# Kernel optimization log

Measured on AMD Instinct MI355X. Metric: run time of the kernel, lower is better.

The kernel has to match this reference:

```python
import math
import jax, jax.numpy as jnp
from jax import lax
import numpy as np

N_IMG = 2
C = 128
IMG_H, IMG_W = 512, 1024
STRIDES = (4, 8, 16, 32, 64)
SIZES = (32.0, 64.0, 128.0, 256.0, 512.0)
RATIOS = (0.5, 1.0, 2.0)
A = len(RATIOS)
PRE_NMS_TOPK = 2000    # pre_nms_topk[self.training] with training=True
POST_NMS_TOPK = 1000   # post_nms_topk[self.training]
NMS_THRESH = 0.7
BATCH_PER_IMG = 256
POS_FRAC = 0.5
MIN_BOX_SIZE = 0.0
SCALE_CLAMP = math.log(1000.0 / 16.0)
MATCH_LOW, MATCH_HIGH = 0.3, 0.7


def cell_anchors(size):
    rs = jnp.asarray(RATIOS, jnp.float32)
    area = size * size
    w = jnp.sqrt(area / rs)
    h = w * rs
    return jnp.stack([-w / 2, -h / 2, w / 2, h / 2], axis=1)  # [A,4]


def level_anchors(H, W, stride, size):
    ca = cell_anchors(size)
    sx = jnp.arange(W, dtype=jnp.float32) * stride
    sy = jnp.arange(H, dtype=jnp.float32) * stride
    yy, xx = jnp.meshgrid(sy, sx, indexing="ij")
    shifts = jnp.stack([xx, yy, xx, yy], axis=-1).reshape(-1, 4)  # [H*W,4]
    return (shifts[:, None, :] + ca[None, :, :]).reshape(-1, 4)  # [H*W*A,4]


def pairwise_iou(a, b):
    lt = jnp.maximum(a[:, None, :2], b[None, :, :2])
    rb = jnp.minimum(a[:, None, 2:], b[None, :, 2:])
    wh = jnp.clip(rb - lt, 0.0)
    inter = wh[..., 0] * wh[..., 1]
    area_a = (a[:, 2] - a[:, 0]) * (a[:, 3] - a[:, 1])
    area_b = (b[:, 2] - b[:, 0]) * (b[:, 3] - b[:, 1])
    union = area_a[:, None] + area_b[None, :] - inter
    return jnp.where(inter > 0, inter / union, 0.0)


def get_deltas(src, tgt):
    sw = src[..., 2] - src[..., 0]; sh = src[..., 3] - src[..., 1]
    scx = src[..., 0] + 0.5 * sw;   scy = src[..., 1] + 0.5 * sh
    tw = tgt[..., 2] - tgt[..., 0]; th = tgt[..., 3] - tgt[..., 1]
    tcx = tgt[..., 0] + 0.5 * tw;   tcy = tgt[..., 1] + 0.5 * th
    return jnp.stack([(tcx - scx) / sw, (tcy - scy) / sh,
                      jnp.log(tw / sw), jnp.log(th / sh)], axis=-1)


def apply_deltas(deltas, boxes):
    w = boxes[..., 2] - boxes[..., 0]; h = boxes[..., 3] - boxes[..., 1]
    cx = boxes[..., 0] + 0.5 * w;      cy = boxes[..., 1] + 0.5 * h
    dx, dy = deltas[..., 0], deltas[..., 1]
    dw = jnp.minimum(deltas[..., 2], SCALE_CLAMP)
    dh = jnp.minimum(deltas[..., 3], SCALE_CLAMP)
    pcx = dx * w + cx; pcy = dy * h + cy
    pw = jnp.exp(dw) * w; ph = jnp.exp(dh) * h
    return jnp.stack([pcx - 0.5 * pw, pcy - 0.5 * ph,
                      pcx + 0.5 * pw, pcy + 0.5 * ph], axis=-1)


def conv(x, w, b):
    y = lax.conv_general_dilated(x, w, (1, 1), "SAME",
                                 dimension_numbers=("NCHW", "OIHW", "NCHW"))
    return y + b[None, :, None, None]


def rpn_forward_flat(feats, conv_w, conv_b, obj_w, obj_b, delta_w, delta_b):
    anchors, logits, deltas = [], [], []
    for (stride, size), f in zip(zip(STRIDES, SIZES), feats):
        N, _, H, W = f.shape
        h = jax.nn.relu(conv(f, conv_w, conv_b))
        lg = conv(h, obj_w, obj_b)       # [N,A,H,W]
        dl = conv(h, delta_w, delta_b)   # [N,4A,H,W]
        logits.append(lg.transpose(0, 2, 3, 1).reshape(N, -1))                     # [N,HWA]
        deltas.append(dl.reshape(N, A, 4, H, W).transpose(0, 3, 4, 1, 2).reshape(N, -1, 4))
        anchors.append(level_anchors(H, W, stride, size))
    return anchors, logits, deltas


def label_and_sample(gt_b, key, anchors_all):
    iou = pairwise_iou(gt_b, anchors_all)                 # [G,R]
    matched_idxs = jnp.argmax(iou, axis=0)
    matched_vals = jnp.max(iou, axis=0)
    labels = jnp.where(matched_vals >= MATCH_HIGH, 1,
             jnp.where(matched_vals >= MATCH_LOW, -1, 0))
    highest = jnp.max(iou, axis=1)                        # per-gt best IoU
    lq = jnp.any((iou == highest[:, None]) & (highest[:, None] > 0), axis=0)
    labels = jnp.where(lq, 1, labels)                     # allow_low_quality_matches
    R = labels.shape[0]
    kf, kb = jax.random.split(key)
    fg = labels == 1; bg = labels == 0
    num_fg = jnp.minimum(fg.sum(), int(POS_FRAC * BATCH_PER_IMG))
    num_bg = jnp.minimum(bg.sum(), BATCH_PER_IMG - num_fg)
    def pick(mask, k, num):
        pri = jnp.where(mask, jax.random.uniform(k, (R,)), jnp.inf)
        rank = jnp.argsort(jnp.argsort(pri))
        return rank < num
    sel_fg = pick(fg, kf, num_fg)
    sel_bg = pick(bg, kb, num_bg)
    labels = jnp.where(sel_fg, 1, jnp.where(sel_bg, 0, -1))
    return labels, gt_b[matched_idxs]


def losses_fn(anchors_all, logits_cat, deltas_cat, gt_labels, matched_gt):
    fg = (gt_labels == 1).astype(logits_cat.dtype)          # [N,R]
    gt_deltas = get_deltas(anchors_all[None], matched_gt)   # [N,R,4]
    loc = jnp.sum(jnp.abs(deltas_cat - gt_deltas) * fg[..., None])  # smooth_l1, beta=0
    valid = (gt_labels >= 0).astype(logits_cat.dtype)
    x = logits_cat
    bce = jnp.maximum(x, 0.0) - x * fg + jnp.log1p(jnp.exp(-jnp.abs(x)))
    cls = jnp.sum(bce * valid)
    norm = float(BATCH_PER_IMG) * logits_cat.shape[0]
    return jnp.stack([cls / norm, loc / norm])


def nms_keep(boxes, valid):
    # boxes are sorted by descending score; greedy suppression.
    K = boxes.shape[0]
    iou = pairwise_iou(boxes, boxes)
    idx = jnp.arange(K)
    def body(i, keep):
        sup = (iou[i] > NMS_THRESH) & (idx > i) & keep[i]
        return keep & ~sup
    return lax.fori_loop(0, K, body, valid)


def predict_proposals(anchors, logits, deltas):
    lvl_boxes, lvl_scores = [], []
    for anc, lg, dl in zip(anchors, logits, deltas):
        boxes = apply_deltas(dl, anc[None])             # [N,R_l,4]
        k = min(PRE_NMS_TOPK, lg.shape[1])
        ts, ti = lax.top_k(lg, k)                       # [N,k]
        tb = jnp.take_along_axis(boxes, ti[..., None], axis=1)
        tb = jnp.stack([jnp.clip(tb[..., 0], 0.0, IMG_W), jnp.clip(tb[..., 1], 0.0, IMG_H),
                        jnp.clip(tb[..., 2], 0.0, IMG_W), jnp.clip(tb[..., 3], 0.0, IMG_H)], -1)
        valid = ((tb[..., 2] - tb[..., 0]) > MIN_BOX_SIZE) & ((tb[..., 3] - tb[..., 1]) > MIN_BOX_SIZE)
        keep = jax.vmap(nms_keep)(tb, valid)
        lvl_boxes.append(tb)
        lvl_scores.append(jnp.where(keep, ts, -jnp.inf))
    all_b = jnp.concatenate(lvl_boxes, axis=1)
    all_s = jnp.concatenate(lvl_scores, axis=1)
    fs, fi = lax.top_k(all_s, POST_NMS_TOPK)
    fb = jnp.take_along_axis(all_b, fi[..., None], axis=1)
    return fb, fs


def setup_inputs() -> dict:
    key = jax.random.key(0)
    ks = jax.random.split(key, 12)
    out = {}
    for i, s in enumerate(STRIDES):
        out[f"feat_p{i+2}"] = jax.random.normal(ks[i], (N_IMG, C, IMG_H // s, IMG_W // s), jnp.float32)
    G = 32
    wh_scale = jnp.asarray([IMG_W, IMG_H], jnp.float32)
    cxy = jax.random.uniform(ks[5], (N_IMG, G, 2)) * wh_scale
    wh = 32.0 + jax.random.uniform(ks[6], (N_IMG, G, 2)) * 224.0
    x1y1 = jnp.clip(cxy - wh / 2, 0.0)
    x2y2 = jnp.maximum(jnp.minimum(cxy + wh / 2, wh_scale), x1y1 + 1.0)
    out["gt_boxes"] = jnp.concatenate([x1y1, x2y2], axis=-1)
    out["conv_w"] = 0.01 * jax.random.normal(ks[7], (C, C, 3, 3), jnp.float32)
    out["conv_b"] = jnp.zeros((C,), jnp.float32)
    out["obj_w"] = 0.01 * jax.random.normal(ks[8], (A, C, 1, 1), jnp.float32)
    out["obj_b"] = jnp.zeros((A,), jnp.float32)
    out["delta_w"] = 0.01 * jax.random.normal(ks[9], (4 * A, C, 1, 1), jnp.float32)
    out["delta_b"] = jnp.zeros((4 * A,), jnp.float32)
    return out


def reference(feat_p2, feat_p3, feat_p4, feat_p5, feat_p6, gt_boxes,
              conv_w, conv_b, obj_w, obj_b, delta_w, delta_b):
    feats = [feat_p2, feat_p3, feat_p4, feat_p5, feat_p6]
    anchors, logits, deltas = rpn_forward_flat(feats, conv_w, conv_b, obj_w, obj_b, delta_w, delta_b)
    anchors_all = jnp.concatenate(anchors, axis=0)      # [R,4]
    logits_cat = jnp.concatenate(logits, axis=1)        # [N,R]
    deltas_cat = jnp.concatenate(deltas, axis=1)        # [N,R,4]
    keys = jax.random.split(jax.random.key(42), gt_boxes.shape[0])
    gt_labels, matched_gt = jax.vmap(label_and_sample, in_axes=(0, 0, None))(gt_boxes, keys, anchors_all)
    losses = losses_fn(anchors_all, logits_cat, deltas_cat, gt_labels, matched_gt)
    prop_boxes, prop_scores = predict_proposals(
        anchors,
        [lax.stop_gradient(l) for l in logits],
        [lax.stop_gradient(d) for d in deltas])
    return prop_boxes, prop_scores, losses
```

## Files before the change

kernel.cpp:

```cpp
#include <hip/hip_runtime.h>
#include <stdint.h>
#include <math.h>


#define R_TOT   130944
#define HALF_R  65472
#define TOTK    7920
#define SCALE_CLAMP 4.135166556742356

__host__ __device__ inline void threefry(uint32_t k0, uint32_t k1,
                                         uint32_t x0, uint32_t x1,
                                         uint32_t* o0, uint32_t* o1)
{
  uint32_t ks[3]; ks[0]=k0; ks[1]=k1; ks[2]=k0^k1^0x1BD11BDAu;
  x0 += ks[0]; x1 += ks[1];
  const uint32_t rot0[4] = {13u,15u,26u,6u};
  const uint32_t rot1[4] = {17u,29u,16u,24u};
  for (int i = 0; i < 5; i++){
    const uint32_t* rot = (i & 1) ? rot1 : rot0;
    for (int q = 0; q < 4; q++){
      x0 += x1;
      x1 = (x1 << rot[q]) | (x1 >> (32u - rot[q]));
      x1 ^= x0;
    }
    x0 += ks[(i+1)%3];
    x1 += ks[(i+2)%3] + (uint32_t)(i+1);
  }
  *o0 = x0; *o1 = x1;
}

__device__ inline unsigned long long mono64(double v){
  unsigned long long b = (unsigned long long)__double_as_longlong(v);
  return (b & 0x8000000000000000ull) ? ~b : (b | 0x8000000000000000ull);
}

__device__ __forceinline__ double iou_cf(double g0,double g1,double g2,double g3,
                                         double a0,double a1,double a2,double a3){
  #pragma clang fp contract(off)
  double lt0 = fmax(g0,a0), lt1 = fmax(g1,a1);
  double rb0 = fmin(g2,a2), rb1 = fmin(g3,a3);
  double w = rb0-lt0; if (w<0.0) w=0.0;
  double h = rb1-lt1; if (h<0.0) h=0.0;
  double inter = w*h;
  double aa = (g2-g0)*(g3-g1);
  double ab = (a2-a0)*(a3-a1);
  double uni = aa+ab-inter;
  return inter>0.0 ? inter/uni : 0.0;
}

__device__ __forceinline__ void anchor_of(int r, double* o){
  #pragma clang fp contract(off)
  const int    base[5]={0,98304,122880,129024,130560};
  const int    Wl[5]  ={256,128,64,32,16};
  const double strd[5]={4.0,8.0,16.0,32.0,64.0};
  const double size[5]={32.0,64.0,128.0,256.0,512.0};
  const double ratio[3]={0.5,1.0,2.0};
  int l=0; while (l<4 && r>=base[l+1]) l++;
  int rr=r-base[l]; int pix=rr/3; int a=rr-pix*3;
  int x=pix%Wl[l], y=pix/Wl[l];
  double w=sqrt(size[l]*size[l]/ratio[a]);
  double h=w*ratio[a];
  double sx=(double)x*strd[l], sy=(double)y*strd[l];
  o[0]=sx-0.5*w; o[1]=sy-0.5*h; o[2]=sx+0.5*w; o[3]=sy+0.5*h;
}

__device__ __forceinline__ void decode_box(int ridx, const double* __restrict__ d,
                                           double* __restrict__ o){
  double a[4]; anchor_of(ridx,a);
  double w=a[2]-a[0], h=a[3]-a[1];
  double cx=a[0]+0.5*w, cy=a[1]+0.5*h;
  double dw=fmin(d[2],SCALE_CLAMP), dh=fmin(d[3],SCALE_CLAMP);
  double pcx=d[0]*w+cx, pcy=d[1]*h+cy;
  double pw=exp(dw)*w, ph=exp(dh)*h;
  double x1=pcx-0.5*pw, y1=pcy-0.5*ph;
  double x2=pcx+0.5*pw, y2=pcy+0.5*ph;
  o[0]=fmin(fmax(x1,0.0),1024.0); o[1]=fmin(fmax(y1,0.0),512.0);
  o[2]=fmin(fmax(x2,0.0),1024.0); o[3]=fmin(fmax(y2,0.0),512.0);
}

__device__ inline void bitonic_desc(double* sv, int* si, int M, int tid, int nthr){
  for (int k=2;k<=M;k<<=1)
    for (int j=k>>1;j>0;j>>=1){
      __syncthreads();
      for (int i=tid;i<M;i+=nthr){
        int ixj=i^j;
        if (ixj>i){
          double va=sv[i], vb=sv[ixj]; int ia=si[i], ib=si[ixj];
          bool before = (va>vb) || (va==vb && ia<ib);
          bool up = ((i&k)==0);
          if (up ? !before : before){ sv[i]=vb; sv[ixj]=va; si[i]=ib; si[ixj]=ia; }
        }
      }
    }
  __syncthreads();
}

__device__ inline void bitonic_asc_u(uint32_t* sk, int* si, int M, int tid, int nthr){
  for (int k=2;k<=M;k<<=1)
    for (int j=k>>1;j>0;j>>=1){
      __syncthreads();
      for (int i=tid;i<M;i+=nthr){
        int ixj=i^j;
        if (ixj>i){
          uint32_t ka=sk[i], kb=sk[ixj]; int ia=si[i], ib=si[ixj];
          bool before = (ka<kb) || (ka==kb && ia<ib);
          bool up = ((i&k)==0);
          if (up ? !before : before){ sk[i]=kb; sk[ixj]=ka; si[i]=ib; si[ixj]=ia; }
        }
      }
    }
  __syncthreads();
}

__global__ __launch_bounds__(256) void k_pre(const float* __restrict__ cw,
    float* __restrict__ cwTf, uint32_t* __restrict__ ub,
    const float* __restrict__ gt, unsigned long long* __restrict__ highest,
    uint32_t kf00,uint32_t kf01,uint32_t kb00,uint32_t kb01,
    uint32_t kf10,uint32_t kf11,uint32_t kb10,uint32_t kb11)
{
  const int bx=blockIdx.x, tid=threadIdx.x;
  if (bx < 576){
    int o = bx*256 + tid;
    if (o >= 147456) return;
    int cc = o & 127; int t = o >> 7;
    int k9 = t % 9;  int ci = t / 9;
    cwTf[(size_t)(ci*9+k9)*128 + cc] = cw[(size_t)cc*1152 + ci*9 + k9];
  } else if (bx < 1599){
    int j = (bx-576)*256 + tid;
    if (j >= 2*R_TOT) return;
    int slot = j / HALF_R; int t = j - slot*HALF_R;
    uint32_t k0,k1;
    if      (slot==0){k0=kf00;k1=kf01;}
    else if (slot==1){k0=kb00;k1=kb01;}
    else if (slot==2){k0=kf10;k1=kf11;}
    else             {k0=kb10;k1=kb11;}
    uint32_t o0,o1;
    threefry(k0,k1,(uint32_t)t,(uint32_t)(t+HALF_R),&o0,&o1);
    ub[(size_t)slot*R_TOT+t]=o0;
    ub[(size_t)slot*R_TOT+t+HALF_R]=o1;
  } else {
    __shared__ double gts[128];
    __shared__ unsigned long long lmax[32];
    const int gb=bx-1599;
    const int img=gb>>6, b=gb&63;
    if (tid<128) gts[tid]=(double)gt[img*128+tid];
    if (tid<32) lmax[tid]=0ull;
    __syncthreads();
    double gm[32];
    #pragma unroll
    for (int g=0;g<32;g++) gm[g]=0.0;
    for (int r=b*256+tid; r<R_TOT; r+=64*256){
      double a[4]; anchor_of(r,a);
      #pragma unroll
      for (int g=0;g<32;g++){
        double v=iou_cf(gts[g*4],gts[g*4+1],gts[g*4+2],gts[g*4+3],a[0],a[1],a[2],a[3]);
        gm[g]=fmax(gm[g],v);
      }
    }
    #pragma unroll
    for (int g=0;g<32;g++){
      double v=gm[g];
      #pragma unroll
      for (int off=1; off<64; off<<=1) v=fmax(v,__shfl_xor(v,off));
      if ((tid&63)==0) atomicMax(&lmax[g],(unsigned long long)__double_as_longlong(v));
    }
    __syncthreads();
    if (tid<32) atomicMax(&highest[img*32+tid], lmax[tid]);
  }
}

#define CTH 4
#define CTW 8

__global__ __launch_bounds__(256,3) void k_conv_label(
    const float* __restrict__ f2, const float* __restrict__ f3,
    const float* __restrict__ f4, const float* __restrict__ f5,
    const float* __restrict__ f6,
    const float* __restrict__ cwTf, const float* __restrict__ cb,
    const float* __restrict__ ow, const float* __restrict__ ob,
    const float* __restrict__ dwt, const float* __restrict__ dbt,
    double* __restrict__ logits, double* __restrict__ dpred,
    const float* __restrict__ gt, const unsigned long long* __restrict__ highest,
    int* __restrict__ prelab, int* __restrict__ matched,
    int* __restrict__ labels, int* __restrict__ counts)
{
  __shared__ double fshd[4][6][12];
  __shared__ __align__(16) char ush[33792];
  float*  wshF = (float*)ush;
  double* hshp = (double*)ush;
  __shared__ float hw[15*128];
  __shared__ float hb[15];

  const int tid=threadIdx.x;

  if (blockIdx.x >= 2728){
    double* gts=(double*)ush;
    double* hg =(double*)(ush+1024);
    int* wfg=(int*)(ush+1280); int* wbg=(int*)(ush+1296);
    const int lb=blockIdx.x-2728;
    const int img=lb>>9, blk=lb&511;
    if (tid<128) gts[tid]=(double)gt[img*128+tid];
    if (tid<32)  hg[tid]=__longlong_as_double((long long)highest[img*32+tid]);
    __syncthreads();
    int r=blk*256+tid;
    const bool ok=(r<R_TOT);
    int lab=-1, bi=0;
    if (ok){
      double a[4]; anchor_of(r,a);
      double best=-1.0; bool lq=false;
      #pragma unroll
      for (int g=0;g<32;g++){
        double v=iou_cf(gts[g*4],gts[g*4+1],gts[g*4+2],gts[g*4+3],a[0],a[1],a[2],a[3]);
        if (v>best){ best=v; bi=g; }
        if (hg[g]>0.0 && v==hg[g]) lq=true;
      }
      lab = lq ? 1 : (best>=0.7 ? 1 : (best>=0.3 ? -1 : 0));
      prelab [(size_t)img*R_TOT+r]=lab;
      matched[(size_t)img*R_TOT+r]=bi;
      labels [(size_t)img*R_TOT+r]=-1;
    }
    unsigned long long bf=__ballot(ok && lab==1);
    unsigned long long bb=__ballot(ok && lab==0);
    const int wid=tid>>6, lane=tid&63;
    if (lane==0){ wfg[wid]=__popcll(bf); wbg[wid]=__popcll(bb); }
    __syncthreads();
    if (tid==0){
      int fcnt=wfg[0]+wfg[1]+wfg[2]+wfg[3];
      int bcnt=wbg[0]+wbg[1]+wbg[2]+wbg[3];
      if (fcnt) atomicAdd(&counts[img*2+0],fcnt);
      if (bcnt) atomicAdd(&counts[img*2+1],bcnt);
    }
    return;
  }

  const int cumt[6]={0,2048,2560,2688,2720,2728};
  const int Hs[5]={128,64,32,16,8}, Wl[5]={256,128,64,32,16};
  const int rbs[5]={0,98304,122880,129024,130560};
  const int lgx[5]={5,4,3,2,1};

  int bid=blockIdx.x;
  int lvl=0;
  while (lvl<4 && bid>=cumt[lvl+1]) lvl++;
  int t=bid-cumt[lvl];
  const int img=t&1; const int tt=t>>1;
  const int H=Hs[lvl], W=Wl[lvl], rbase=rbs[lvl];
  const int tx=tt&((1<<lgx[lvl])-1), ty=tt>>lgx[lvl];
  const int x0=tx*CTW, y0=ty*CTH;
  const float* f = lvl==0?f2: lvl==1?f3: lvl==2?f4: lvl==3?f5: f6;

  for (int i=tid;i<15*128;i+=256){
    int o=i>>7, c=i&127;
    hw[i]=(o<3)?ow[o*128+c]:dwt[(o-3)*128+c];
  }
  if (tid<15) hb[tid]=(tid<3)?ob[tid]:dbt[tid-3];

  const int c=tid&127, half=tid>>7;
  double acc[16];
  #pragma unroll
  for (int i=0;i<16;i++) acc[i]=0.0;

  const float* fimg = f + (size_t)img*128*H*W;

  const bool fin_act = (tid < 240);
  int ci_f=0,dy_f=0,dx_f=0; bool fin_valid=false;
  const float* fptr=fimg;
  if (fin_act){
    ci_f=tid/60; int rem=tid-ci_f*60; dy_f=rem/10; dx_f=rem-dy_f*10;
    int y=y0-1+dy_f, x=x0-1+dx_f;
    fin_valid = (y>=0&&y<H&&x>=0&&x<W);
    fptr = fimg + (size_t)ci_f*H*W + (fin_valid ? ((size_t)y*W+x) : 0);
  }
  const size_t fstep=(size_t)4*H*W;
  const float2* wsrc=(const float2*)cwTf;

  float fin_pf=0.f; float2 wpf[9];
  if (fin_act){ fin_pf = fin_valid ? *fptr : 0.f; fptr += fstep; }
  #pragma unroll
  for (int j2=0;j2<9;j2++) wpf[j2]=wsrc[tid+j2*256];

  for (int ci0=0; ci0<128; ci0+=4){
    __syncthreads();
    if (fin_act) fshd[ci_f][dy_f][dx_f]=(double)fin_pf;
    { float2* wdst=(float2*)wshF;
      #pragma unroll
      for (int j2=0;j2<9;j2++) wdst[tid+j2*256]=wpf[j2]; }
    if (ci0+4<128){
      if (fin_act){ fin_pf = fin_valid ? *fptr : 0.f; fptr += fstep; }
      const float2* wn = wsrc + (size_t)(ci0+4)*576;
      #pragma unroll
      for (int j2=0;j2<9;j2++) wpf[j2]=wn[tid+j2*256];
    }
    __syncthreads();
    #pragma unroll
    for (int ci=0;ci<4;ci++){
      double w9d[9];
      #pragma unroll
      for (int k=0;k<9;k++) w9d[k]=(double)wshF[(ci*9+k)*128 + c];
      #pragma unroll
      for (int irl=0;irl<4;irl++){
        int ir=half*2+irl;
        double rowb[10];
        #pragma unroll
        for (int q=0;q<10;q++) rowb[q]=fshd[ci][ir][q];
        #pragma unroll
        for (int orl=0;orl<2;orl++){
          int ky=irl-orl;
          if (ky<0||ky>2) continue;
          #pragma unroll
          for (int px=0;px<8;px++){
            double s=acc[orl*8+px];
            #pragma unroll
            for (int kx=0;kx<3;kx++) s += w9d[ky*3+kx]*rowb[px+kx];
            acc[orl*8+px]=s;
          }
        }
      }
    }
  }
  __syncthreads();
  double bc=(double)cb[c];
  #pragma unroll
  for (int pp=0;pp<16;pp++){
    double hv=acc[pp]+bc; if (hv<0.0) hv=0.0;
    hshp[c*33+(half*16+pp)]=hv;
  }
  __syncthreads();
  for (int j=tid;j<480;j+=256){
    int o=j>>5, p=j&31;
    int py=p>>3, px=p&7;
    double s=(double)hb[o];
    for (int c2=0;c2<128;c2++) s += (double)hw[o*128+c2]*hshp[c2*33+p];
    int gy=y0+py, gx=x0+px;
    long long pix=(long long)gy*W+gx;
    size_t rb=(size_t)rbase+(size_t)pix*3;
    if (o<3) logits[(size_t)img*R_TOT+rb+o]=s;
    else { int a=(o-3)>>2, jj=(o-3)&3; dpred[((size_t)img*R_TOT+rb+a)*4+jj]=s; }
  }
}

__global__ __launch_bounds__(1024) void k_mid2(const uint32_t* __restrict__ ub,
    const int* __restrict__ prelab, const int* __restrict__ counts,
    int* __restrict__ labels,
    const double* __restrict__ logits, const double* __restrict__ dpred,
    double* __restrict__ allS, double* __restrict__ allB)
{
  __shared__ __align__(16) char buf[49152];
  __shared__ int hist[256];
  __shared__ int sI0, sI1; __shared__ unsigned long long sT;
  __shared__ int cnt;
  const int tid=threadIdx.x;

  if (blockIdx.x < 4){
    uint32_t* skey=(uint32_t*)buf; int* sidx=(int*)(buf+16384);
    const int img=blockIdx.x>>1, cls=blockIdx.x&1;
    const int cfg=counts[img*2+0], cbg=counts[img*2+1];
    const int num_fg=cfg<128?cfg:128;
    const int cap_bg=256-num_fg;
    const int num=cls?(cbg<cap_bg?cbg:cap_bg):num_fg;
    if (num<=0) return;
    const int want=cls?0:1;
    const int sel=want;
    const uint32_t* u=ub+(size_t)(img*2+cls)*R_TOT;
    const int* pl=prelab+(size_t)img*R_TOT;
    int* lab=labels+(size_t)img*R_TOT;

    for (int b=tid;b<256;b+=1024) hist[b]=0;
    if (tid==0) cnt=0;
    __syncthreads();
    for (int r=tid;r<R_TOT;r+=1024){
      int plr = pl[r];
      uint32_t key = u[r]>>9;
      if (plr==want) atomicAdd(&hist[key>>15],1);
    }
    __syncthreads();
    if (tid==0){
      int cum=0,b=0;
      for (;b<255;b++){ int hh=hist[b]; if (cum+hh>=num) break; cum+=hh; }
      sI0=b; sI1=num-cum;
    }
    __syncthreads();
    const uint32_t bsel=(uint32_t)sI0; const int kneed=sI1;
    for (int r=tid;r<R_TOT;r+=1024){
      int plr = pl[r];
      uint32_t key = u[r]>>9;
      if (plr==want){
        uint32_t t8=key>>15;
        if (t8<bsel) lab[r]=sel;
        else if (t8==bsel){ int p=atomicAdd(&cnt,1); if (p<4096){ skey[p]=key; sidx[p]=r; } }
      }
    }
    __syncthreads();
    int n=cnt<4096?cnt:4096;
    for (int i=tid;i<4096;i+=1024) if (i>=n){ skey[i]=0xFFFFFFFFu; sidx[i]=0x7FFFFFFF; }
    bitonic_asc_u(skey,sidx,4096,tid,1024);
    int take = kneed<n?kneed:n;
    for (int i=tid;i<take;i+=1024) lab[sidx[i]]=sel;
  } else {
    double* sv=(double*)buf; int* si=(int*)(buf+32768);
    const int Rl[5]   ={98304,24576,6144,1536,384};
    const int kl[5]   ={2000,2000,2000,1536,384};
    const int lbase[5]={0,98304,122880,129024,130560};
    const int loff[5] ={0,2000,4000,6000,7536};
    const int bb=blockIdx.x-4;
    const int lvl=bb%5, img=bb/5;
    const int Rn=Rl[lvl], K=kl[lvl];
    const double* lg=logits+(size_t)img*R_TOT+lbase[lvl];

    unsigned long long chosen=0; int kneed=K;
    for (int ps=7; ps>=6; --ps){
      int shift=ps*8;
      for (int b=tid;b<256;b+=1024) hist[b]=0;
      __syncthreads();
      for (int r=tid;r<Rn;r+=1024){
        unsigned long long ik=~mono64(lg[r]);
        bool okp=(ps==7)||((ik>>(shift+8))==(chosen>>(shift+8)));
        if (okp) atomicAdd(&hist[(int)((ik>>shift)&255)],1);
      }
      __syncthreads();
      if (tid==0){
        int cum=0,b=0;
        for (;b<255;b++){ int hh=hist[b]; if (cum+hh>=kneed) break; cum+=hh; }
        sT=chosen|((unsigned long long)b<<shift); sI1=kneed-cum;
      }
      __syncthreads();
      chosen=sT; kneed=sI1;
      __syncthreads();
    }
    const unsigned long long lim = chosen | 0xFFFFFFFFFFFFull;
    if (tid==0) cnt=0;
    __syncthreads();
    for (int r=tid;r<Rn;r+=1024){
      unsigned long long ik=~mono64(lg[r]);
      if (ik<=lim){ int p=atomicAdd(&cnt,1); if (p<4096){ sv[p]=lg[r]; si[p]=r; } }
    }
    __syncthreads();
    int n=cnt<4096?cnt:4096;
    for (int i=tid;i<4096;i+=1024) if (i>=n){ sv[i]=-HUGE_VAL; si[i]=0x7FFFFFFF; }
    bitonic_desc(sv,si,4096,tid,1024);
    for (int j=tid;j<K;j+=1024){
      double v=sv[j]; int r=si[j];
      size_t slot=(size_t)img*TOTK+loff[lvl]+j;
      allS[slot]=v;
      int ridx=lbase[lvl]+r;
      double bx[4];
      decode_box(ridx, dpred+((size_t)img*R_TOT+ridx)*4, bx);
      allB[slot*4+0]=bx[0]; allB[slot*4+1]=bx[1]; allB[slot*4+2]=bx[2]; allB[slot*4+3]=bx[3];
    }
  }
}

__global__ __launch_bounds__(256) void k_mid3(const double* __restrict__ allB,
    unsigned long long* __restrict__ msk,
    const double* __restrict__ logits, const double* __restrict__ dpred,
    const float* __restrict__ gt, const int* __restrict__ labels,
    const int* __restrict__ matched, double* __restrict__ part)
{
  const int bx=blockIdx.x, tid=threadIdx.x;
  if (bx < 1980){
    __shared__ double Bsh[8000];
    const int kl[5]  ={2000,2000,2000,1536,384};
    const int loff[5]={0,2000,4000,6000,7536};
    const int rbc[6] ={0,250,500,750,942,990};
    const int img = bx/990; int t = bx - img*990;
    int lvl=0; while (lvl<4 && t>=rbc[lvl+1]) lvl++;
    const int i0=(t-rbc[lvl])*8;
    const int K=kl[lvl]; const int nw=(K+63)>>6;
    const double* B=allB+(size_t)(img*TOTK+loff[lvl])*4;
    for (int q=tid;q<K*4;q+=256) Bsh[q]=B[q];
    __syncthreads();
    const int wv=tid>>6, lane=tid&63;
    for (int rr=0;rr<8;rr++){
      int i=i0+rr;
      if (i>=K) break;
      const double bi0=Bsh[i*4],bi1=Bsh[i*4+1],bi2=Bsh[i*4+2],bi3=Bsh[i*4+3];
      const double areai=(bi2-bi0)*(bi3-bi1);
      for (int w=wv;w<nw;w+=4){
        int j=w*64+lane;
        bool pred=false;
        if (j<K && j>i){
          double a0=Bsh[j*4],a1=Bsh[j*4+1],a2=Bsh[j*4+2],a3=Bsh[j*4+3];
          double lt0=fmax(bi0,a0), lt1=fmax(bi1,a1);
          double rb0=fmin(bi2,a2), rb1=fmin(bi3,a3);
          double ww=rb0-lt0; if (ww<0.0) ww=0.0;
          double hh=rb1-lt1; if (hh<0.0) hh=0.0;
          double inter=ww*hh;
          double uni=areai+(a2-a0)*(a3-a1)-inter;
          double iou=inter>0.0?inter/uni:0.0;
          pred = iou>0.7;
        }
        unsigned long long m=__ballot(pred);
        if (lane==0) msk[((size_t)img*TOTK+loff[lvl]+i)*32+w]=m;
      }
    }
  } else {
    const int bid2=bx-1980;
    double cls=0.0, loc=0.0;
    for (int idx=bid2*256+tid; idx<2*R_TOT; idx+=256*256){
      int l=labels[idx];
      if (l<0) continue;
      double x=logits[idx];
      double fgv=(l==1)?1.0:0.0;
      cls += fmax(x,0.0)-x*fgv+log1p(exp(-fabs(x)));
      if (l==1){
        int img=idx/R_TOT, r=idx-img*R_TOT;
        double a[4]; anchor_of(r,a);
        int m=matched[idx];
        const float* g=gt+img*128+m*4;
        double sw=a[2]-a[0], sh=a[3]-a[1];
        double scx=a[0]+0.5*sw, scy=a[1]+0.5*sh;
        double tw=(double)g[2]-(double)g[0], th=(double)g[3]-(double)g[1];
        double tcx=(double)g[0]+0.5*tw, tcy=(double)g[1]+0.5*th;
        double d0=(tcx-scx)/sw, d1=(tcy-scy)/sh;
        double d2=log(tw/sw), d3=log(th/sh);
        const double* dp=dpred+(size_t)idx*4;
        loc += fabs(dp[0]-d0)+fabs(dp[1]-d1)+fabs(dp[2]-d2)+fabs(dp[3]-d3);
      }
    }
    __shared__ double sc[256], sl[256];
    sc[tid]=cls; sl[tid]=loc; __syncthreads();
    for (int s=128;s>0;s>>=1){
      if (tid<s){ sc[tid]+=sc[tid+s]; sl[tid]+=sl[tid+s]; }
      __syncthreads();
    }
    if (tid==0){ part[bid2*2]=sc[0]; part[bid2*2+1]=sl[0]; }
  }
}

#define NMS_LD(BUF, BASE) do{ \
  _Pragma("unroll") \
  for (int j_=0;j_<16;j_++){ int i_=(BASE)+j_; \
    BUF[j_] = (lane<nw && i_<K) ? M[(size_t)i_*32+lane] : 0ull; } \
}while(0)
#define NMS_PR(BUF, BASE) do{ \
  _Pragma("unroll") \
  for (int j_=0;j_<16;j_++){ int i_=(BASE)+j_; \
    if (i_<K){ unsigned long long kw_=__shfl(keep,(i_>>6)); \
      if ((kw_>>(i_&63))&1ull) keep &= ~BUF[j_]; } } \
}while(0)

__global__ void k_nmsscan(const double* __restrict__ allB, double* __restrict__ allS,
    const unsigned long long* __restrict__ msk){
  const int kl[5]  ={2000,2000,2000,1536,384};
  const int loff[5]={0,2000,4000,6000,7536};
  const int lvl=blockIdx.x, img=blockIdx.y;
  const int K=kl[lvl], off=loff[lvl], nw=(K+63)>>6;
  const int lane=threadIdx.x;
  const double* B=allB+(size_t)(img*TOTK+off)*4;
  const unsigned long long* M=msk+((size_t)img*TOTK+off)*32;
  unsigned long long keep=0ull;
  if (lane<nw){
    for (int b=0;b<64;b++){
      int j=lane*64+b;
      if (j<K){
        double x1=B[(size_t)j*4],y1=B[(size_t)j*4+1],x2=B[(size_t)j*4+2],y2=B[(size_t)j*4+3];
        if ((x2-x1)>0.0 && (y2-y1)>0.0) keep|=(1ull<<b);
      }
    }
  }
  unsigned long long Abuf[16], Bbuf[16];
  NMS_LD(Abuf, 0);
  for (int base=0; base<K; base+=32){
    NMS_LD(Bbuf, base+16);
    NMS_PR(Abuf, base);
    NMS_LD(Abuf, base+32);
    NMS_PR(Bbuf, base+16);
  }
  if (lane<nw){
    for (int b=0;b<64;b++){
      int j=lane*64+b;
      if (j<K && !((keep>>b)&1ull))
        allS[(size_t)img*TOTK+off+j]=-HUGE_VAL;
    }
  }
}

__global__ __launch_bounds__(1024) void k_final(const double* __restrict__ allS,
    const double* __restrict__ allB, const double* __restrict__ part,
    float* __restrict__ out){
  const int tid=threadIdx.x;
  if (blockIdx.x==2){
    __shared__ double sc[256], sl[256];
    if (tid<256){ sc[tid]=part[tid*2]; sl[tid]=part[tid*2+1]; }
    __syncthreads();
    for (int s=128;s>0;s>>=1){
      if (tid<s){ sc[tid]+=sc[tid+s]; sl[tid]+=sl[tid+s]; }
      __syncthreads();
    }
    if (tid==0){ out[10000]=(float)(sc[0]/512.0); out[10001]=(float)(sl[0]/512.0); }
    return;
  }
  const int img=blockIdx.x;
  const double* sarr=allS+(size_t)img*TOTK;
  __shared__ int hist[256];
  __shared__ unsigned long long sT; __shared__ int sK;
  __shared__ double sv[4096]; __shared__ int si[4096]; __shared__ int cnt;

  unsigned long long chosen=0; int kneed=1000;
  for (int ps=7; ps>=0; --ps){
    int shift=ps*8;
    for (int b=tid;b<256;b+=1024) hist[b]=0;
    __syncthreads();
    for (int r=tid;r<TOTK;r+=1024){
      unsigned long long ik=~mono64(sarr[r]);
      bool okp=(ps==7)||((ik>>(shift+8))==(chosen>>(shift+8)));
      if (okp) atomicAdd(&hist[(int)((ik>>shift)&255)],1);
    }
    __syncthreads();
    if (tid==0){
      int cum=0,b=0;
      for (;b<255;b++){ int hh=hist[b]; if (cum+hh>=kneed) break; cum+=hh; }
      sT=chosen|((unsigned long long)b<<shift); sK=kneed-cum;
    }
    __syncthreads();
    chosen=sT; kneed=sK;
    __syncthreads();
  }
  if (tid==0) cnt=0;
  __syncthreads();
  for (int r=tid;r<TOTK;r+=1024){
    unsigned long long ik=~mono64(sarr[r]);
    if (ik<=chosen){ int p=atomicAdd(&cnt,1); if (p<4096){ sv[p]=sarr[r]; si[p]=r; } }
  }
  __syncthreads();
  int n=cnt<4096?cnt:4096;
  for (int i=tid;i<4096;i+=1024) if (i>=n){ sv[i]=-HUGE_VAL; si[i]=0x7FFFFFFF; }
  bitonic_desc(sv,si,4096,tid,1024);
  for (int j=tid;j<1000;j+=1024){
    out[8000+img*1000+j]=(float)sv[j];
    int idx=si[j];
    const double* b=allB+((size_t)img*TOTK+idx)*4;
    float* ob=out+((size_t)img*1000+j)*4;
    ob[0]=(float)b[0]; ob[1]=(float)b[1]; ob[2]=(float)b[2]; ob[3]=(float)b[3];
  }
}

extern "C" void kernel_launch(void* const* d_in, const int* in_sizes, int n_in,
                              void* d_out, int out_size, void* d_ws, size_t ws_size,
                              hipStream_t stream)
{
  (void)in_sizes; (void)n_in; (void)out_size;
  const float* feats[5];
  for (int i=0;i<5;i++) feats[i]=(const float*)d_in[i];
  const float* gt =(const float*)d_in[5];
  const float* cw =(const float*)d_in[6];
  const float* cb =(const float*)d_in[7];
  const float* ow =(const float*)d_in[8];
  const float* ob =(const float*)d_in[9];
  const float* dwt=(const float*)d_in[10];
  const float* dbt=(const float*)d_in[11];
  float* out=(float*)d_out;

  char* p=(char*)d_ws;
  auto carve=[&](size_t nbytes)->char*{ char* q=p; p += (nbytes+255)&~(size_t)255; return q; };
  double* logits =(double*)carve(2ull*R_TOT*8);
  double* dpred  =(double*)carve(2ull*R_TOT*4*8);
  float* cwTf    =(float*)carve(147456ull*4);
  uint32_t* ub   =(uint32_t*)carve(4ull*R_TOT*4);
  int* prelab    =(int*)carve(2ull*R_TOT*4);
  int* matched   =(int*)carve(2ull*R_TOT*4);
  int* labels    =(int*)carve(2ull*R_TOT*4);
  unsigned long long* highest=(unsigned long long*)carve(2*32*8);
  int* counts    =(int*)carve(256);
  double* allS   =(double*)carve(2ull*TOTK*8);
  double* allB   =(double*)carve(2ull*TOTK*4*8);
  unsigned long long* msk=(unsigned long long*)carve(2ull*TOTK*32*8);
  double* part   =(double*)carve(256*2*8);
  if ((size_t)(p-(char*)d_ws) > ws_size) return;

  hipMemsetAsync(highest, 0, 768, stream);

  uint32_t a0,b0,a1,b1;
  threefry(0u,42u,0u,2u,&a0,&b0);
  threefry(0u,42u,1u,3u,&a1,&b1);
  uint32_t kf00,kf01,kb00,kb01,kf10,kf11,kb10,kb11;
  { uint32_t c0,d0,c1,d1;
    threefry(a0,a1,0u,2u,&c0,&d0); threefry(a0,a1,1u,3u,&c1,&d1);
    kf00=c0; kf01=c1; kb00=d0; kb01=d1;
    threefry(b0,b1,0u,2u,&c0,&d0); threefry(b0,b1,1u,3u,&c1,&d1);
    kf10=c0; kf11=c1; kb10=d0; kb11=d1; }

  k_pre<<<1727, 256, 0, stream>>>(cw, cwTf, ub, gt, highest,
      kf00,kf01,kb00,kb01,kf10,kf11,kb10,kb11);
  k_conv_label<<<3752, 256, 0, stream>>>(feats[0],feats[1],feats[2],feats[3],feats[4],
      cwTf,cb,ow,ob,dwt,dbt, logits, dpred,
      gt, highest, prelab, matched, labels, counts);
  k_mid2<<<14, 1024, 0, stream>>>(ub, prelab, counts, labels, logits, dpred, allS, allB);
  k_mid3<<<2236, 256, 0, stream>>>(allB, msk, logits, dpred, gt, labels, matched, part);
  k_nmsscan<<<dim3(5,2), 64, 0, stream>>>(allB, allS, msk);
  k_final<<<3, 1024, 0, stream>>>(allS, allB, part, out);
}
```

Before: 1.424 ms.

## Read conv weights directly from a padded per-channel layout and halve conv LDS

The conv weights are now transposed into a per-output-channel layout padded to 12 floats, so each thread reads its 3x3 weights straight from global or cache with float4 loads instead of staging them through shared memory every 4 input channels. The hidden-activation buffer is cut in half by writing and consuming the two pixel halves in turn, which roughly halves shared memory and raises launch bounds to 4 blocks per CU. The threefry random-bit generation moves from k_pre into extra blocks of the conv kernel. The cost is more global/L1 weight traffic per thread and an extra barrier and serialized head pass in the epilogue.

```diff
diff --git a/kernel.cpp b/kernel.cpp
--- a/kernel.cpp
+++ b/kernel.cpp
@@ -113,20 +113,75 @@
 }
 
 __global__ __launch_bounds__(256) void k_pre(const float* __restrict__ cw,
-    float* __restrict__ cwTf, uint32_t* __restrict__ ub,
-    const float* __restrict__ gt, unsigned long long* __restrict__ highest,
+    float* __restrict__ cwTf, const float* __restrict__ gt,
+    unsigned long long* __restrict__ highest)
+{
+  const int bx=blockIdx.x, tid=threadIdx.x;
+  if (bx < 768){
+    int o = bx*256 + tid;
+    if (o >= 147456) return;
+    int cc = o / 1152; int rem = o - cc*1152;
+    int ci = rem / 9;  int k9 = rem - ci*9;
+    cwTf[((size_t)cc*128 + ci)*12 + k9] = cw[o];
+  } else {
+    __shared__ double gts[128];
+    __shared__ unsigned long long lmax[32];
+    const int gb=bx-768;
+    const int img=gb>>6, b=gb&63;
+    if (tid<128) gts[tid]=(double)gt[img*128+tid];
+    if (tid<32) lmax[tid]=0ull;
+    __syncthreads();
+    double gm[32];
+    #pragma unroll
+    for (int g=0;g<32;g++) gm[g]=0.0;
+    for (int r=b*256+tid; r<R_TOT; r+=64*256){
+      double a[4]; anchor_of(r,a);
+      #pragma unroll
+      for (int g=0;g<32;g++){
+        double v=iou_cf(gts[g*4],gts[g*4+1],gts[g*4+2],gts[g*4+3],a[0],a[1],a[2],a[3]);
+        gm[g]=fmax(gm[g],v);
+      }
+    }
+    #pragma unroll
+    for (int g=0;g<32;g++){
+      double v=gm[g];
+      #pragma unroll
+      for (int off=1; off<64; off<<=1) v=fmax(v,__shfl_xor(v,off));
+      if ((tid&63)==0) atomicMax(&lmax[g],(unsigned long long)__double_as_longlong(v));
+    }
+    __syncthreads();
+    if (tid<32) atomicMax(&highest[img*32+tid], lmax[tid]);
+  }
+}
+
+#define CTH 4
+#define CTW 8
+
+__global__ __launch_bounds__(256,4) void k_conv_label(
+    const float* __restrict__ f2, const float* __restrict__ f3,
+    const float* __restrict__ f4, const float* __restrict__ f5,
+    const float* __restrict__ f6,
+    const float* __restrict__ cwTf, const float* __restrict__ cb,
+    const float* __restrict__ ow, const float* __restrict__ ob,
+    const float* __restrict__ dwt, const float* __restrict__ dbt,
+    double* __restrict__ logits, double* __restrict__ dpred,
+    const float* __restrict__ gt, const unsigned long long* __restrict__ highest,
+    int* __restrict__ prelab, int* __restrict__ matched,
+    int* __restrict__ labels, int* __restrict__ counts,
+    uint32_t* __restrict__ ub,
     uint32_t kf00,uint32_t kf01,uint32_t kb00,uint32_t kb01,
     uint32_t kf10,uint32_t kf11,uint32_t kb10,uint32_t kb11)
 {
-  const int bx=blockIdx.x, tid=threadIdx.x;
-  if (bx < 576){
-    int o = bx*256 + tid;
-    if (o >= 147456) return;
-    int cc = o & 127; int t = o >> 7;
-    int k9 = t % 9;  int ci = t / 9;
-    cwTf[(size_t)(ci*9+k9)*128 + cc] = cw[(size_t)cc*1152 + ci*9 + k9];
-  } else if (bx < 1599){
-    int j = (bx-576)*256 + tid;
+  __shared__ double fshd[4][6][12];
+  __shared__ __align__(16) char ush[17408];
+  double* hshp = (double*)ush;
+  __shared__ float hw[15*128];
+  __shared__ float hb[15];
+
+  const int tid=threadIdx.x;
+
+  if (blockIdx.x >= 3752){
+    int j = (blockIdx.x-3752)*256 + tid;
     if (j >= 2*R_TOT) return;
     int slot = j / HALF_R; int t = j - slot*HALF_R;
     uint32_t k0,k1;
@@ -138,60 +193,8 @@
     threefry(k0,k1,(uint32_t)t,(uint32_t)(t+HALF_R),&o0,&o1);
     ub[(size_t)slot*R_TOT+t]=o0;
     ub[(size_t)slot*R_TOT+t+HALF_R]=o1;
-  } else {
-    __shared__ double gts[128];
-    __shared__ unsigned long long lmax[32];
-    const int gb=bx-1599;
-    const int img=gb>>6, b=gb&63;
-    if (tid<128) gts[tid]=(double)gt[img*128+tid];
-    if (tid<32) lmax[tid]=0ull;
-    __syncthreads();
-    double gm[32];
-    #pragma unroll
-    for (int g=0;g<32;g++) gm[g]=0.0;
-    for (int r=b*256+tid; r<R_TOT; r+=64*256){
-      double a[4]; anchor_of(r,a);
-      #pragma unroll
-      for (int g=0;g<32;g++){
-        double v=iou_cf(gts[g*4],gts[g*4+1],gts[g*4+2],gts[g*4+3],a[0],a[1],a[2],a[3]);
-        gm[g]=fmax(gm[g],v);
-      }
-    }
-    #pragma unroll
-    for (int g=0;g<32;g++){
-      double v=gm[g];
-      #pragma unroll
-      for (int off=1; off<64; off<<=1) v=fmax(v,__shfl_xor(v,off));
-      if ((tid&63)==0) atomicMax(&lmax[g],(unsigned long long)__double_as_longlong(v));
-    }
-    __syncthreads();
-    if (tid<32) atomicMax(&highest[img*32+tid], lmax[tid]);
-  }
-}
-
-#define CTH 4
-#define CTW 8
-
-__global__ __launch_bounds__(256,3) void k_conv_label(
-    const float* __restrict__ f2, const float* __restrict__ f3,
-    const float* __restrict__ f4, const float* __restrict__ f5,
-    const float* __restrict__ f6,
-    const float* __restrict__ cwTf, const float* __restrict__ cb,
-    const float* __restrict__ ow, const float* __restrict__ ob,
-    const float* __restrict__ dwt, const float* __restrict__ dbt,
-    double* __restrict__ logits, double* __restrict__ dpred,
-    const float* __restrict__ gt, const unsigned long long* __restrict__ highest,
-    int* __restrict__ prelab, int* __restrict__ matched,
-    int* __restrict__ labels, int* __restrict__ counts)
-{
-  __shared__ double fshd[4][6][12];
-  __shared__ __align__(16) char ush[33792];
-  float*  wshF = (float*)ush;
-  double* hshp = (double*)ush;
-  __shared__ float hw[15*128];
-  __shared__ float hb[15];
-
-  const int tid=threadIdx.x;
+    return;
+  }
 
   if (blockIdx.x >= 2728){
     double* gts=(double*)ush;
@@ -260,6 +263,7 @@
   for (int i=0;i<16;i++) acc[i]=0.0;
 
   const float* fimg = f + (size_t)img*128*H*W;
+  const float* wbase = cwTf + (size_t)c*1536;
 
   const bool fin_act = (tid < 240);
   int ci_f=0,dy_f=0,dx_f=0; bool fin_valid=false;
@@ -271,31 +275,25 @@
     fptr = fimg + (size_t)ci_f*H*W + (fin_valid ? ((size_t)y*W+x) : 0);
   }
   const size_t fstep=(size_t)4*H*W;
-  const float2* wsrc=(const float2*)cwTf;
-
-  float fin_pf=0.f; float2 wpf[9];
+
+  float fin_pf=0.f;
   if (fin_act){ fin_pf = fin_valid ? *fptr : 0.f; fptr += fstep; }
-  #pragma unroll
-  for (int j2=0;j2<9;j2++) wpf[j2]=wsrc[tid+j2*256];
 
   for (int ci0=0; ci0<128; ci0+=4){
     __syncthreads();
     if (fin_act) fshd[ci_f][dy_f][dx_f]=(double)fin_pf;
-    { float2* wdst=(float2*)wshF;
-      #pragma unroll
-      for (int j2=0;j2<9;j2++) wdst[tid+j2*256]=wpf[j2]; }
     if (ci0+4<128){
       if (fin_act){ fin_pf = fin_valid ? *fptr : 0.f; fptr += fstep; }
-      const float2* wn = wsrc + (size_t)(ci0+4)*576;
-      #pragma unroll
-      for (int j2=0;j2<9;j2++) wpf[j2]=wn[tid+j2*256];
     }
     __syncthreads();
     #pragma unroll
     for (int ci=0;ci<4;ci++){
+      const float4* wp=(const float4*)(wbase + (size_t)(ci0+ci)*12);
+      float4 wA=wp[0], wB=wp[1], wC=wp[2];
       double w9d[9];
-      #pragma unroll
-      for (int k=0;k<9;k++) w9d[k]=(double)wshF[(ci*9+k)*128 + c];
+      w9d[0]=(double)wA.x; w9d[1]=(double)wA.y; w9d[2]=(double)wA.z; w9d[3]=(double)wA.w;
+      w9d[4]=(double)wB.x; w9d[5]=(double)wB.y; w9d[6]=(double)wB.z; w9d[7]=(double)wB.w;
+      w9d[8]=(double)wC.x;
       #pragma unroll
       for (int irl=0;irl<4;irl++){
         int ir=half*2+irl;
@@ -317,24 +315,40 @@
       }
     }
   }
+  double bc=(double)cb[c];
   __syncthreads();
-  double bc=(double)cb[c];
-  #pragma unroll
-  for (int pp=0;pp<16;pp++){
-    double hv=acc[pp]+bc; if (hv<0.0) hv=0.0;
-    hshp[c*33+(half*16+pp)]=hv;
+  if (half==0){
+    #pragma unroll
+    for (int pp=0;pp<16;pp++){
+      double hv=acc[pp]+bc; if (hv<0.0) hv=0.0;
+      hshp[c*17+pp]=hv;
+    }
   }
   __syncthreads();
-  for (int j=tid;j<480;j+=256){
-    int o=j>>5, p=j&31;
-    int py=p>>3, px=p&7;
-    double s=(double)hb[o];
-    for (int c2=0;c2<128;c2++) s += (double)hw[o*128+c2]*hshp[c2*33+p];
-    int gy=y0+py, gx=x0+px;
-    long long pix=(long long)gy*W+gx;
-    size_t rb=(size_t)rbase+(size_t)pix*3;
-    if (o<3) logits[(size_t)img*R_TOT+rb+o]=s;
-    else { int a=(o-3)>>2, jj=(o-3)&3; dpred[((size_t)img*R_TOT+rb+a)*4+jj]=s; }
+  for (int hp=0;hp<2;hp++){
+    if (tid<240){
+      int o=tid>>4, p=tid&15;
+      double s=(double)hb[o];
+      for (int c2=0;c2<128;c2++) s += (double)hw[o*128+c2]*hshp[c2*17+p];
+      int pg=hp*16+p;
+      int py=pg>>3, px=pg&7;
+      int gy=y0+py, gx=x0+px;
+      long long pix=(long long)gy*W+gx;
+      size_t rb=(size_t)rbase+(size_t)pix*3;
+      if (o<3) logits[(size_t)img*R_TOT+rb+o]=s;
+      else { int a=(o-3)>>2, jj=(o-3)&3; dpred[((size_t)img*R_TOT+rb+a)*4+jj]=s; }
+    }
+    if (hp==0){
+      __syncthreads();
+      if (half==1){
+        #pragma unroll
+        for (int pp=0;pp<16;pp++){
+          double hv=acc[pp]+bc; if (hv<0.0) hv=0.0;
+          hshp[c*17+pp]=hv;
+        }
+      }
+      __syncthreads();
+    }
   }
 }
 
@@ -654,7 +668,7 @@
   auto carve=[&](size_t nbytes)->char*{ char* q=p; p += (nbytes+255)&~(size_t)255; return q; };
   double* logits =(double*)carve(2ull*R_TOT*8);
   double* dpred  =(double*)carve(2ull*R_TOT*4*8);
-  float* cwTf    =(float*)carve(147456ull*4);
+  float* cwTf    =(float*)carve(128ull*128*12*4);
   uint32_t* ub   =(uint32_t*)carve(4ull*R_TOT*4);
   int* prelab    =(int*)carve(2ull*R_TOT*4);
   int* matched   =(int*)carve(2ull*R_TOT*4);
@@ -679,11 +693,11 @@
     threefry(b0,b1,0u,2u,&c0,&d0); threefry(b0,b1,1u,3u,&c1,&d1);
     kf10=c0; kf11=c1; kb10=d0; kb11=d1; }
 
-  k_pre<<<1727, 256, 0, stream>>>(cw, cwTf, ub, gt, highest,
-      kf00,kf01,kb00,kb01,kf10,kf11,kb10,kb11);
-  k_conv_label<<<3752, 256, 0, stream>>>(feats[0],feats[1],feats[2],feats[3],feats[4],
+  k_pre<<<896, 256, 0, stream>>>(cw, cwTf, gt, highest);
+  k_conv_label<<<4775, 256, 0, stream>>>(feats[0],feats[1],feats[2],feats[3],feats[4],
       cwTf,cb,ow,ob,dwt,dbt, logits, dpred,
-      gt, highest, prelab, matched, labels, counts);
+      gt, highest, prelab, matched, labels, counts,
+      ub, kf00,kf01,kb00,kb01,kf10,kf11,kb10,kb11);
   k_mid2<<<14, 1024, 0, stream>>>(ub, prelab, counts, labels, logits, dpred, allS, allB);
   k_mid3<<<2236, 256, 0, stream>>>(allB, msk, logits, dpred, gt, labels, matched, part);
   k_nmsscan<<<dim3(5,2), 64, 0, stream>>>(allB, allS, msk);
```

Result: slower. 1.467 ms (+3.0%).
